# Kernel tuning notes

Hardware: AMD Instinct MI355X
Metric: run time of the kernel (lower is better)

The kernel has to match this reference:

```python
import jax, jax.numpy as jnp
import numpy as np


def setup_inputs() -> dict:
    key = jax.random.key(0)
    k1, k2 = jax.random.split(key)
    set1 = jax.random.normal(k1, (8192, 256), dtype=jnp.float32)
    set2 = jax.random.normal(k2, (8192, 256), dtype=jnp.float32)
    return {"set1": set1, "set2": set2}


def reference(set1, set2):
    # Pairwise Euclidean distances via the Gram trick:
    sq1 = jnp.sum(set1 * set1, axis=-1)  # [N]
    sq2 = jnp.sum(set2 * set2, axis=-1)  # [M]
    gram = jnp.einsum('nd,md->nm', set1, set2)  # [N,M]
    d2 = sq1[:, None] + sq2[None, :] - 2.0 * gram
    d = jnp.sqrt(jnp.maximum(d2, 0.0))  # clamp tiny negatives from roundoff
    term_1 = jnp.mean(jnp.min(d, axis=1))  # for each point in set1, nearest in set2
    term_2 = jnp.mean(jnp.min(d, axis=0))  # for each point in set2, nearest in set1
    return term_1 + term_2
```

## Files before the change

### kernel.cpp

```cpp
#include <hip/hip_runtime.h>

#define N_PTS 8192
#define D_DIM 256
#define BN 256
#define BM 128
#define BK 64
#define NBLK ((N_PTS / BN) * (N_PTS / BM))
#define INF_BITS 0x7F800000u

typedef __attribute__((ext_vector_type(8))) short short8;
typedef __attribute__((ext_vector_type(4))) float f32x4;

__device__ __forceinline__ void gload_lds16(const ushort* g, ushort* l) {
    __builtin_amdgcn_global_load_lds(
        (const __attribute__((address_space(1))) void*)g,
        (__attribute__((address_space(3))) void*)l, 16, 0, 0);
}

__device__ __forceinline__ ushort f2bf(float x) {
    unsigned u = __float_as_uint(x);
    return (ushort)((u + 0x7FFFu + ((u >> 16) & 1u)) >> 16);
}

__global__ void prep_kernel(const float* __restrict__ s1, const float* __restrict__ s2,
                            ushort* __restrict__ b1, ushort* __restrict__ b2,
                            float* __restrict__ sq1, float* __restrict__ sq2,
                            unsigned* __restrict__ rowmin2, unsigned* __restrict__ colmin2,
                            unsigned* __restrict__ counter) {
    const int half = N_PTS * D_DIM;
    int t = blockIdx.x * 256 + threadIdx.x;
    int e = t * 8;
    bool first = e < half;
    const float* src = first ? s1 : s2;
    ushort* dst = first ? b1 : b2;
    int off = first ? e : e - half;
    float4 v0 = *(const float4*)(src + off);
    float4 v1 = *(const float4*)(src + off + 4);
    float s = v0.x * v0.x + v0.y * v0.y + v0.z * v0.z + v0.w * v0.w
            + v1.x * v1.x + v1.y * v1.y + v1.z * v1.z + v1.w * v1.w;
    ushort4 o0 = { f2bf(v0.x), f2bf(v0.y), f2bf(v0.z), f2bf(v0.w) };
    ushort4 o1 = { f2bf(v1.x), f2bf(v1.y), f2bf(v1.z), f2bf(v1.w) };
    *(ushort4*)(dst + off)     = o0;
    *(ushort4*)(dst + off + 4) = o1;
    #pragma unroll
    for (int m = 1; m <= 16; m <<= 1) s += __shfl_xor(s, m, 64);
    int sub = threadIdx.x & 31;
    int row = off >> 8;
    if (sub == 0) (first ? sq1 : sq2)[row] = s;
    if (sub == 1) (first ? rowmin2 : colmin2)[row] = INF_BITS;
    if (t == 0) *counter = 0;
}

__global__ __launch_bounds__(256, 2) void tile_kernel(
    const ushort* __restrict__ B1, const ushort* __restrict__ B2,
    const float* __restrict__ sq1, const float* __restrict__ sq2,
    unsigned* __restrict__ rowmin2, unsigned* __restrict__ colmin2,
    unsigned* __restrict__ counter, float* __restrict__ out) {
    __shared__ ushort As[BN * BK] __attribute__((aligned(16)));
    __shared__ ushort Bs[BM * BK] __attribute__((aligned(16)));
    __shared__ unsigned rs[BN];
    __shared__ unsigned cs[BM];
    __shared__ unsigned s_old;
    __shared__ float wsum[4];

    const int tid  = threadIdx.x;
    const int lane = tid & 63;
    const int w    = tid >> 6;
    const int quad = lane >> 4;
    const int c    = lane & 15;
    const int n_off = (w >> 1) * 128;
    const int m_off = (w & 1) * 64;
    const int n0 = blockIdx.y * BN;
    const int m0 = blockIdx.x * BM;

    rs[tid] = INF_BITS;
    if (tid < BM) cs[tid] = INF_BITS;

    f32x4 acc[8][4];
    #pragma unroll
    for (int ti = 0; ti < 8; ti++)
        #pragma unroll
        for (int tj = 0; tj < 4; tj++) acc[ti][tj] = (f32x4){0.f, 0.f, 0.f, 0.f};

    for (int k0 = 0; k0 < D_DIM; k0 += BK) {
        #pragma unroll
        for (int r = 0; r < 8; r++) {
            int idx = r * 256 + tid;
            int row = idx >> 3;
            int gc  = (idx & 7) ^ (row & 7);
            gload_lds16(B1 + (size_t)(n0 + row) * D_DIM + k0 + gc * 8,
                        &As[(idx & ~63) * 8]);
        }
        #pragma unroll
        for (int r = 0; r < 4; r++) {
            int idx = r * 256 + tid;
            int row = idx >> 3;
            int gc  = (idx & 7) ^ (row & 7);
            gload_lds16(B2 + (size_t)(m0 + row) * D_DIM + k0 + gc * 8,
                        &Bs[(idx & ~63) * 8]);
        }
        __syncthreads();

        #pragma unroll
        for (int kk = 0; kk < 2; kk++) {
            short8 a[8], b[4];
            #pragma unroll
            for (int ti = 0; ti < 8; ti++) {
                int row = n_off + ti * 16 + c;
                int ch  = (kk * 4 + quad) ^ (row & 7);
                a[ti] = *(const short8*)&As[row * BK + ch * 8];
            }
            #pragma unroll
            for (int tj = 0; tj < 4; tj++) {
                int row = m_off + tj * 16 + c;
                int ch  = (kk * 4 + quad) ^ (row & 7);
                b[tj] = *(const short8*)&Bs[row * BK + ch * 8];
            }
            #pragma unroll
            for (int ti = 0; ti < 8; ti++)
                #pragma unroll
                for (int tj = 0; tj < 4; tj++)
                    acc[ti][tj] = __builtin_amdgcn_mfma_f32_16x16x32_bf16(
                        a[ti], b[tj], acc[ti][tj], 0, 0, 0);
        }
        __syncthreads();
    }

    float sqm[4];
    #pragma unroll
    for (int tj = 0; tj < 4; tj++) sqm[tj] = sq2[m0 + m_off + tj * 16 + c];
    float cmin[4];
    #pragma unroll
    for (int tj = 0; tj < 4; tj++) cmin[tj] = __uint_as_float(INF_BITS);

    #pragma unroll
    for (int ti = 0; ti < 8; ti++) {
        float4 sqn = *(const float4*)&sq1[n0 + n_off + ti * 16 + quad * 4];
        float snr[4] = { sqn.x, sqn.y, sqn.z, sqn.w };
        float rmin[4] = { __uint_as_float(INF_BITS), __uint_as_float(INF_BITS),
                          __uint_as_float(INF_BITS), __uint_as_float(INF_BITS) };
        #pragma unroll
        for (int tj = 0; tj < 4; tj++)
            #pragma unroll
            for (int r = 0; r < 4; r++) {
                float d2 = fmaxf(snr[r] + sqm[tj] - 2.f * acc[ti][tj][r], 0.f);
                rmin[r]  = fminf(rmin[r], d2);
                cmin[tj] = fminf(cmin[tj], d2);
            }
        #pragma unroll
        for (int m = 1; m <= 8; m <<= 1)
            #pragma unroll
            for (int r = 0; r < 4; r++)
                rmin[r] = fminf(rmin[r], __shfl_xor(rmin[r], m, 64));
        if (c == 0) {
            #pragma unroll
            for (int r = 0; r < 4; r++)
                atomicMin(&rs[n_off + ti * 16 + quad * 4 + r], __float_as_uint(rmin[r]));
        }
    }
    #pragma unroll
    for (int m = 16; m <= 32; m <<= 1)
        #pragma unroll
        for (int tj = 0; tj < 4; tj++)
            cmin[tj] = fminf(cmin[tj], __shfl_xor(cmin[tj], m, 64));
    if (quad == 0) {
        #pragma unroll
        for (int tj = 0; tj < 4; tj++)
            atomicMin(&cs[m_off + tj * 16 + c], __float_as_uint(cmin[tj]));
    }
    __syncthreads();

    atomicMin(&rowmin2[n0 + tid], rs[tid]);
    if (tid < BM) atomicMin(&colmin2[m0 + tid], cs[tid]);

    __syncthreads();
    if (tid == 0)
        s_old = __hip_atomic_fetch_add(counter, 1u, __ATOMIC_RELAXED,
                                       __HIP_MEMORY_SCOPE_AGENT);
    __syncthreads();
    if (s_old == NBLK - 1) {
        const unsigned* mins = rowmin2;
        float s = 0.f;
        #pragma unroll 1
        for (int j = 0; j < 64; j += 8) {
            unsigned v[8];
            #pragma unroll
            for (int q = 0; q < 8; q++)
                v[q] = __hip_atomic_load(&mins[(j + q) * 256 + tid],
                                         __ATOMIC_RELAXED, __HIP_MEMORY_SCOPE_AGENT);
            #pragma unroll
            for (int q = 0; q < 8; q++) s += sqrtf(__uint_as_float(v[q]));
        }
        #pragma unroll
        for (int m = 32; m > 0; m >>= 1) s += __shfl_xor(s, m, 64);
        if (lane == 0) wsum[w] = s;
        __syncthreads();
        if (tid == 0) out[0] = (wsum[0] + wsum[1] + wsum[2] + wsum[3]) / (float)N_PTS;
    }
}

extern "C" void kernel_launch(void* const* d_in, const int* in_sizes, int n_in,
                              void* d_out, int out_size, void* d_ws, size_t ws_size,
                              hipStream_t stream) {
    const float* set1 = (const float*)d_in[0];
    const float* set2 = (const float*)d_in[1];
    float* out = (float*)d_out;

    unsigned* rowmin2 = (unsigned*)d_ws;
    unsigned* colmin2 = rowmin2 + N_PTS;
    float* sq1 = (float*)(colmin2 + N_PTS);
    float* sq2 = sq1 + N_PTS;
    unsigned* counter = (unsigned*)(sq2 + N_PTS);
    ushort* b1 = (ushort*)((char*)d_ws + 128 * 1024);
    ushort* b2 = b1 + (size_t)N_PTS * D_DIM;

    prep_kernel<<<(2 * N_PTS * D_DIM) / (256 * 8), 256, 0, stream>>>(
        set1, set2, b1, b2, sq1, sq2, rowmin2, colmin2, counter);
    tile_kernel<<<dim3(N_PTS / BM, N_PTS / BN), 256, 0, stream>>>(
        b1, b2, sq1, sq2, rowmin2, colmin2, counter, out);
}
```

Baseline: 123.0 us.

## Switch Gram matrix computation from bf16 to fp8 MFMA

Converts both input sets to fp8 (packed conversion) instead of bf16 in the prep kernel. The tile kernel loads fp8 tiles into half-size LDS buffers with a new swizzle and uses 16x16x32 fp8 MFMA. Occupancy hint rises to 3 blocks per CU. The aim is to halve memory and LDS traffic and use the faster fp8 path. The cost is much lower precision in the dot products, which could disturb nearest-neighbour distances beyond tolerance.

```diff
diff --git a/kernel.cpp b/kernel.cpp
--- a/kernel.cpp
+++ b/kernel.cpp
@@ -8,22 +8,16 @@
 #define NBLK ((N_PTS / BN) * (N_PTS / BM))
 #define INF_BITS 0x7F800000u
 
-typedef __attribute__((ext_vector_type(8))) short short8;
 typedef __attribute__((ext_vector_type(4))) float f32x4;
 
-__device__ __forceinline__ void gload_lds16(const ushort* g, ushort* l) {
+__device__ __forceinline__ void gload_lds16(const unsigned char* g, unsigned char* l) {
     __builtin_amdgcn_global_load_lds(
         (const __attribute__((address_space(1))) void*)g,
         (__attribute__((address_space(3))) void*)l, 16, 0, 0);
 }
 
-__device__ __forceinline__ ushort f2bf(float x) {
-    unsigned u = __float_as_uint(x);
-    return (ushort)((u + 0x7FFFu + ((u >> 16) & 1u)) >> 16);
-}
-
 __global__ void prep_kernel(const float* __restrict__ s1, const float* __restrict__ s2,
-                            ushort* __restrict__ b1, ushort* __restrict__ b2,
+                            unsigned char* __restrict__ f1, unsigned char* __restrict__ f2,
                             float* __restrict__ sq1, float* __restrict__ sq2,
                             unsigned* __restrict__ rowmin2, unsigned* __restrict__ colmin2,
                             unsigned* __restrict__ counter) {
@@ -32,16 +26,17 @@
     int e = t * 8;
     bool first = e < half;
     const float* src = first ? s1 : s2;
-    ushort* dst = first ? b1 : b2;
+    unsigned char* dst = first ? f1 : f2;
     int off = first ? e : e - half;
     float4 v0 = *(const float4*)(src + off);
     float4 v1 = *(const float4*)(src + off + 4);
     float s = v0.x * v0.x + v0.y * v0.y + v0.z * v0.z + v0.w * v0.w
             + v1.x * v1.x + v1.y * v1.y + v1.z * v1.z + v1.w * v1.w;
-    ushort4 o0 = { f2bf(v0.x), f2bf(v0.y), f2bf(v0.z), f2bf(v0.w) };
-    ushort4 o1 = { f2bf(v1.x), f2bf(v1.y), f2bf(v1.z), f2bf(v1.w) };
-    *(ushort4*)(dst + off)     = o0;
-    *(ushort4*)(dst + off + 4) = o1;
+    int p0 = __builtin_amdgcn_cvt_pk_fp8_f32(v0.x, v0.y, 0, false);
+    p0     = __builtin_amdgcn_cvt_pk_fp8_f32(v0.z, v0.w, p0, true);
+    int p1 = __builtin_amdgcn_cvt_pk_fp8_f32(v1.x, v1.y, 0, false);
+    p1     = __builtin_amdgcn_cvt_pk_fp8_f32(v1.z, v1.w, p1, true);
+    *(int2*)(dst + off) = make_int2(p0, p1);
     #pragma unroll
     for (int m = 1; m <= 16; m <<= 1) s += __shfl_xor(s, m, 64);
     int sub = threadIdx.x & 31;
@@ -51,13 +46,13 @@
     if (t == 0) *counter = 0;
 }
 
-__global__ __launch_bounds__(256, 2) void tile_kernel(
-    const ushort* __restrict__ B1, const ushort* __restrict__ B2,
+__global__ __launch_bounds__(256, 3) void tile_kernel(
+    const unsigned char* __restrict__ F1, const unsigned char* __restrict__ F2,
     const float* __restrict__ sq1, const float* __restrict__ sq2,
     unsigned* __restrict__ rowmin2, unsigned* __restrict__ colmin2,
     unsigned* __restrict__ counter, float* __restrict__ out) {
-    __shared__ ushort As[BN * BK] __attribute__((aligned(16)));
-    __shared__ ushort Bs[BM * BK] __attribute__((aligned(16)));
+    __shared__ unsigned char As[BN * BK] __attribute__((aligned(16)));
+    __shared__ unsigned char Bs[BM * BK] __attribute__((aligned(16)));
     __shared__ unsigned rs[BN];
     __shared__ unsigned cs[BM];
     __shared__ unsigned s_old;
@@ -84,43 +79,43 @@
 
     for (int k0 = 0; k0 < D_DIM; k0 += BK) {
         #pragma unroll
-        for (int r = 0; r < 8; r++) {
-            int idx = r * 256 + tid;
-            int row = idx >> 3;
-            int gc  = (idx & 7) ^ (row & 7);
-            gload_lds16(B1 + (size_t)(n0 + row) * D_DIM + k0 + gc * 8,
-                        &As[(idx & ~63) * 8]);
-        }
-        #pragma unroll
         for (int r = 0; r < 4; r++) {
             int idx = r * 256 + tid;
-            int row = idx >> 3;
-            int gc  = (idx & 7) ^ (row & 7);
-            gload_lds16(B2 + (size_t)(m0 + row) * D_DIM + k0 + gc * 8,
-                        &Bs[(idx & ~63) * 8]);
+            int row = idx >> 2;
+            int gc  = (idx & 3) ^ ((row >> 1) & 3);
+            gload_lds16(F1 + (size_t)(n0 + row) * D_DIM + k0 + gc * 16,
+                        &As[(idx & ~63) * 16]);
+        }
+        #pragma unroll
+        for (int r = 0; r < 2; r++) {
+            int idx = r * 256 + tid;
+            int row = idx >> 2;
+            int gc  = (idx & 3) ^ ((row >> 1) & 3);
+            gload_lds16(F2 + (size_t)(m0 + row) * D_DIM + k0 + gc * 16,
+                        &Bs[(idx & ~63) * 16]);
         }
         __syncthreads();
 
         #pragma unroll
         for (int kk = 0; kk < 2; kk++) {
-            short8 a[8], b[4];
+            long a[8], b[4];
             #pragma unroll
             for (int ti = 0; ti < 8; ti++) {
-                int row = n_off + ti * 16 + c;
-                int ch  = (kk * 4 + quad) ^ (row & 7);
-                a[ti] = *(const short8*)&As[row * BK + ch * 8];
+                int row  = n_off + ti * 16 + c;
+                int slot = (kk * 2 + (quad >> 1)) ^ ((row >> 1) & 3);
+                a[ti] = *(const long*)&As[row * BK + slot * 16 + (quad & 1) * 8];
             }
             #pragma unroll
             for (int tj = 0; tj < 4; tj++) {
-                int row = m_off + tj * 16 + c;
-                int ch  = (kk * 4 + quad) ^ (row & 7);
-                b[tj] = *(const short8*)&Bs[row * BK + ch * 8];
+                int row  = m_off + tj * 16 + c;
+                int slot = (kk * 2 + (quad >> 1)) ^ ((row >> 1) & 3);
+                b[tj] = *(const long*)&Bs[row * BK + slot * 16 + (quad & 1) * 8];
             }
             #pragma unroll
             for (int ti = 0; ti < 8; ti++)
                 #pragma unroll
                 for (int tj = 0; tj < 4; tj++)
-                    acc[ti][tj] = __builtin_amdgcn_mfma_f32_16x16x32_bf16(
+                    acc[ti][tj] = __builtin_amdgcn_mfma_f32_16x16x32_fp8_fp8(
                         a[ti], b[tj], acc[ti][tj], 0, 0, 0);
         }
         __syncthreads();
@@ -211,11 +206,11 @@
     float* sq1 = (float*)(colmin2 + N_PTS);
     float* sq2 = sq1 + N_PTS;
     unsigned* counter = (unsigned*)(sq2 + N_PTS);
-    ushort* b1 = (ushort*)((char*)d_ws + 128 * 1024);
-    ushort* b2 = b1 + (size_t)N_PTS * D_DIM;
+    unsigned char* f1 = (unsigned char*)d_ws + 128 * 1024;
+    unsigned char* f2 = f1 + (size_t)N_PTS * D_DIM;
 
     prep_kernel<<<(2 * N_PTS * D_DIM) / (256 * 8), 256, 0, stream>>>(
-        set1, set2, b1, b2, sq1, sq2, rowmin2, colmin2, counter);
+        set1, set2, f1, f2, sq1, sq2, rowmin2, colmin2, counter);
     tile_kernel<<<dim3(N_PTS / BM, N_PTS / BN), 256, 0, stream>>>(
-        b1, b2, sq1, sq2, rowmin2, colmin2, counter, out);
-}
+        f1, f2, sq1, sq2, rowmin2, colmin2, counter, out);
+}
```

Measured after the change: 124.3 us. About the same (+1.0%).
